# Performance work log

Hardware: AMD Instinct MI355X
Metric: run time of the kernel (lower is better)

## Reference

```python
import jax, jax.numpy as jnp
import numpy as np

N_NODES = 100000
N_EDGES = 1200000
NFEAT, NHID, NCLASS = 64, 256, 40
DROP_RATE = 0.5
ORDER = 8


def setup_inputs() -> dict:
    key = jax.random.key(0)
    k = jax.random.split(key, 6)
    x = jax.random.normal(k[0], (N_NODES, NFEAT), dtype=jnp.float32)
    edge_index = jax.random.randint(k[1], (2, N_EDGES), 0, N_NODES, dtype=jnp.int64)
    stdv1 = 1.0 / np.sqrt(NHID)
    stdv2 = 1.0 / np.sqrt(NCLASS)
    W1 = jax.random.normal(k[2], (NFEAT, NHID), dtype=jnp.float32) * stdv1
    b1 = jax.random.normal(k[3], (NHID,), dtype=jnp.float32) * stdv1
    W2 = jax.random.normal(k[4], (NHID, NCLASS), dtype=jnp.float32) * stdv2
    b2 = jax.random.normal(k[5], (NCLASS,), dtype=jnp.float32) * stdv2
    return {"x": x, "edge_index": edge_index, "W1": W1, "b1": b1, "W2": W2, "b2": b2}


def _norm_adj(edge_index, n):
    # A + I, then D^{-1/2} (A+I) D^{-1/2}  (GCN symmetric normalization)
    loops = jnp.arange(n, dtype=edge_index.dtype)
    row = jnp.concatenate([edge_index[0], loops])
    col = jnp.concatenate([edge_index[1], loops])
    ones = jnp.ones(row.shape[0], dtype=jnp.float32)
    deg = jax.ops.segment_sum(ones, row, num_segments=n)  # row sums (self-loops guarantee deg>=1)
    d_inv_sqrt = 1.0 / jnp.sqrt(deg)
    ew = d_inv_sqrt[row] * d_inv_sqrt[col]  # [E+N] edge weights
    return row, col, ew


def reference(x, edge_index, W1, b1, W2, b2):
    n = x.shape[0]
    row, col, ew = _norm_adj(edge_index, n)

    def spmm(h):  # out[row] += ew * h[col]
        return jax.ops.segment_sum(ew[:, None] * h[col], row, num_segments=n)

    # eval-mode input scaling (training=False branch of GRAND.forward)
    h = x * (1.0 - DROP_RATE)
    y = h
    for _ in range(ORDER):
        h = spmm(h)
        y = y + h
    y = y / (ORDER + 1.0)

    # MLP in eval mode: dropouts are no-ops, use_bn=False
    hid = jax.nn.relu(y @ W1 + b1)
    return hid @ W2 + b2
```

## Files before the change

kernel.cpp:

```cpp
#include <hip/hip_runtime.h>

#define NN 100000
#define NE 1200000
#define NF 64
#define NH 256
#define NC 40
#define ORDER_C 8
#define BINB 1024
#define BCAP 165000
#define NSB 782
#define SBROWS 128
#define SBCAP 1920
#define NLB 100
#define CCAP (NE + 7 * NN)

typedef __attribute__((ext_vector_type(8))) short short8;
typedef __attribute__((ext_vector_type(4))) float f32x4;

__device__ __forceinline__ unsigned bf16r(float x) {
    unsigned u = __float_as_uint(x);
    return (u + 0x7FFFu + ((u >> 16) & 1u)) >> 16;
}
__device__ __forceinline__ unsigned packbf(float lo, float hi) {
    return bf16r(lo) | (bf16r(hi) << 16);
}
__device__ __forceinline__ float bflo(unsigned u) { return __uint_as_float(u << 16); }
__device__ __forceinline__ float bfhi(unsigned u) { return __uint_as_float(u & 0xFFFF0000u); }


static __global__ __launch_bounds__(256) void k_bin(const int* __restrict__ rows,
                                                    const int* __restrict__ cols,
                                                    int* __restrict__ bcnt,
                                                    int* __restrict__ browb,
                                                    int* __restrict__ bcolb, int E)
{
    __shared__ int rbuf[BINB];
    __shared__ unsigned short lofs[BINB];
    __shared__ int hist[8], basew[8];
    int t = threadIdx.x;
    int e0 = blockIdx.x * BINB;
    int m = E - e0; if (m > BINB) m = BINB;
    if (t < 8) hist[t] = 0;
    __syncthreads();
    for (int i = t; i < m; i += 256) {
        int r = rows[e0 + i];
        rbuf[i] = r;
        int b = r / 12500;
        lofs[i] = (unsigned short)atomicAdd(&hist[b], 1);
    }
    __syncthreads();
    if (t < 8) basew[t] = atomicAdd(&bcnt[t], hist[t]);
    __syncthreads();
    for (int i = t; i < m; i += 256) {
        int r = rbuf[i];
        int b = r / 12500;
        size_t pos = (size_t)b * BCAP + basew[b] + lofs[i];
        browb[pos] = r;
        bcolb[pos] = cols[e0 + i];
    }
}


static __global__ __launch_bounds__(256) void k_bin98(const int* __restrict__ browb,
                                                      const int* __restrict__ bcolb,
                                                      const int* __restrict__ bcnt,
                                                      int* __restrict__ sbcnt,
                                                      int* __restrict__ sbrow,
                                                      int* __restrict__ sbcol)
{
    __shared__ int rbuf[2048];
    __shared__ unsigned short lofs[2048];
    __shared__ int hist[NLB], basew[NLB];
    int t = threadIdx.x;
    int b = blockIdx.x & 7;
    int m = bcnt[b];
    int lo_sb = (b * 12500) >> 7;
    const int* srcr = browb + (size_t)b * BCAP;
    const int* srcc = bcolb + (size_t)b * BCAP;
    int stride = (gridDim.x >> 3) * 2048;
    for (int base = (blockIdx.x >> 3) * 2048; base < m; base += stride) {
        int cm = m - base; if (cm > 2048) cm = 2048;
        if (t < NLB) hist[t] = 0;
        __syncthreads();
        for (int i = t; i < cm; i += 256) {
            int r = srcr[base + i];
            rbuf[i] = r;
            lofs[i] = (unsigned short)atomicAdd(&hist[(r >> 7) - lo_sb], 1);
        }
        __syncthreads();
        if (t < NLB) {
            int h = hist[t];
            basew[t] = h ? atomicAdd(&sbcnt[lo_sb + t], h) : 0;
        }
        __syncthreads();
        for (int i = t; i < cm; i += 256) {
            int r = rbuf[i];
            int sb = r >> 7;
            int pos = sb * SBCAP + basew[sb - lo_sb] + lofs[i];
            sbrow[pos] = r;
            sbcol[pos] = srcc[base + i];
        }
        __syncthreads();
    }
}


static __global__ __launch_bounds__(256) void k_hist(const int* __restrict__ sbrow,
                                                     const int* __restrict__ sbcnt,
                                                     int* __restrict__ ghist,
                                                     int* __restrict__ sbtot)
{
    __shared__ int h[SBROWS];
    __shared__ int red[256];
    int sb = blockIdx.x;
    int t = threadIdx.x;
    int m = sbcnt[sb];
    const int* src = sbrow + (size_t)sb * SBCAP;
    if (t < SBROWS) h[t] = 0;
    __syncthreads();
    for (int i = t; i < m; i += 256) atomicAdd(&h[src[i] & 127], 1);
    __syncthreads();
    int pad = 0;
    if (t < SBROWS) {
        ghist[sb * SBROWS + t] = h[t];
        pad = (h[t] + 7) & ~7;
    }
    red[t] = pad;
    __syncthreads();
    for (int off = 128; off > 0; off >>= 1) {
        if (t < off) red[t] += red[t + off];
        __syncthreads();
    }
    if (t == 0) sbtot[sb] = red[0];
}


static __global__ __launch_bounds__(1024) void k_scansb(const int* __restrict__ sbtot,
                                                        int* __restrict__ sbbase,
                                                        int* __restrict__ rp, int n)
{
    __shared__ int red[1024];
    int t = threadIdx.x;
    int v = (t < NSB) ? sbtot[t] : 0;
    red[t] = v;
    __syncthreads();
    for (int off = 1; off < 1024; off <<= 1) {
        int x = (t >= off) ? red[t - off] : 0;
        __syncthreads();
        red[t] += x;
        __syncthreads();
    }
    if (t < NSB) sbbase[t] = (t == 0) ? 0 : red[t - 1];
    if (t == NSB - 1) rp[n] = red[t];
}


static __global__ __launch_bounds__(256) void k_csr(const int* __restrict__ sbrow,
                                                    const int* __restrict__ sbcol,
                                                    const int* __restrict__ sbcnt,
                                                    const int* __restrict__ ghist,
                                                    const int* __restrict__ sbbase,
                                                    int* __restrict__ rp,
                                                    float2* __restrict__ drd,
                                                    int* __restrict__ ccol, int n)
{
    __shared__ int rb[SBCAP];
    __shared__ int cb[SBCAP];
    __shared__ int sc[SBROWS], ro[SBROWS], fl[SBROWS];
    int sb = blockIdx.x;
    int t = threadIdx.x;
    int m = sbcnt[sb];
    const int* srcr = sbrow + (size_t)sb * SBCAP;
    const int* srcc = sbcol + (size_t)sb * SBCAP;
    for (int i = t; i < m; i += 256) { rb[i] = srcr[i] & 127; cb[i] = srcc[i]; }
    int h = (t < SBROWS) ? ghist[sb * SBROWS + t] : 0;
    if (t < SBROWS) { sc[t] = (h + 7) & ~7; fl[t] = 0; }
    __syncthreads();
    for (int off = 1; off < SBROWS; off <<= 1) {
        int x = (t >= off && t < SBROWS) ? sc[t - off] : 0;
        __syncthreads();
        if (t < SBROWS) sc[t] += x;
        __syncthreads();
    }
    int base = sbbase[sb];
    if (t < SBROWS) {
        ro[t] = (t == 0) ? 0 : sc[t - 1];
        int row = sb * SBROWS + t;
        if (row < n) {
            rp[row] = base + ro[t];
            float d1 = rsqrtf((float)(h + 1));
            drd[row] = make_float2(d1, (float)(h + 1) * d1);
            int p = (h + 7) & ~7;
            for (int q = h; q < p; ++q) ccol[base + ro[t] + q] = n;
        }
    }
    __syncthreads();
    for (int i = t; i < m; i += 256) {
        int r = rb[i];
        int rank = atomicAdd(&fl[r], 1);
        ccol[base + ro[r] + rank] = cb[i];
    }
}


static __global__ __launch_bounds__(256) void k_pack(const float* __restrict__ W1,
                                                     const float* __restrict__ W2,
                                                     unsigned short* __restrict__ w1f,
                                                     unsigned short* __restrict__ w2f)
{
    int t = blockIdx.x * 256 + threadIdx.x;
    if (t < 2048) {
        int lane = t & 63;
        int g = lane >> 4, col = (lane & 15) + ((t >> 6) & 15) * 16;
        int s = t >> 10;
        unsigned short* p = w1f + (size_t)t * 8;
        #pragma unroll
        for (int e = 0; e < 8; ++e) {
            int k = 32 * s + 8 * g + e;
            p[e] = (unsigned short)bf16r(W1[k * NH + col]);
        }
    } else if (t < 2048 + 1536) {
        int u = t - 2048;
        int lane = u & 63;
        int tile = u >> 6;
        int nt = tile % 3, s = tile / 3;
        int g = lane >> 4, col = (lane & 15) + nt * 16;
        unsigned short* p = w2f + (size_t)u * 8;
        #pragma unroll
        for (int e = 0; e < 8; ++e) {
            int k = 32 * s + 8 * g + e;
            p[e] = (col < NC) ? (unsigned short)bf16r(W2[k * NC + col]) : 0;
        }
    }
}


static __global__ __launch_bounds__(256) void k_init(const float4* __restrict__ x4,
                                                     float4* __restrict__ y4,
                                                     uint4* __restrict__ ga,
                                                     uint4* __restrict__ gbp,
                                                     const float2* __restrict__ drd,
                                                     int nchunk)
{
    int i = blockIdx.x * 256 + threadIdx.x;
    if (i >= nchunk) {
        if (i < nchunk + 8) {
            uint4 z = make_uint4(0, 0, 0, 0);
            ga[i] = z; gbp[i] = z;
        }
        return;
    }
    float d1 = drd[i >> 3].x;
    float4 a = x4[i * 2], b = x4[i * 2 + 1];
    a.x *= 0.5f; a.y *= 0.5f; a.z *= 0.5f; a.w *= 0.5f;
    b.x *= 0.5f; b.y *= 0.5f; b.z *= 0.5f; b.w *= 0.5f;
    y4[i * 2] = a; y4[i * 2 + 1] = b;
    ga[i] = make_uint4(packbf(a.x * d1, a.y * d1), packbf(a.z * d1, a.w * d1),
                       packbf(b.x * d1, b.y * d1), packbf(b.z * d1, b.w * d1));
}


template<bool ACC, bool WRITEG>
static __global__ __launch_bounds__(256) void k_spmm(const uint2* __restrict__ gb,
                                                     uint2* __restrict__ go,
                                                     float4* __restrict__ y4,
                                                     const int* __restrict__ rp,
                                                     const int* __restrict__ ccol,
                                                     const float2* __restrict__ drd, int n)
{
    int wid  = (blockIdx.x * 256 + threadIdx.x) >> 6;
    int lane = threadIdx.x & 63;
    int row  = wid * 4 + (lane >> 4);
    int j    = lane & 15;
    if (row >= n) return;
    int s = rp[row], e = rp[row + 1];

    float a0 = 0.f, a1 = 0.f, a2 = 0.f, a3 = 0.f;
    float b0 = 0.f, b1 = 0.f, b2 = 0.f, b3 = 0.f;
    for (int i = s; i < e; i += 8) {
        int4 cA = *(const int4*)&ccol[i];
        int4 cB = *(const int4*)&ccol[i + 4];
        uint2 h0 = gb[(size_t)cA.x * 16 + j];
        uint2 h1 = gb[(size_t)cA.y * 16 + j];
        uint2 h2 = gb[(size_t)cA.z * 16 + j];
        uint2 h3 = gb[(size_t)cA.w * 16 + j];
        uint2 h4 = gb[(size_t)cB.x * 16 + j];
        uint2 h5 = gb[(size_t)cB.y * 16 + j];
        uint2 h6 = gb[(size_t)cB.z * 16 + j];
        uint2 h7 = gb[(size_t)cB.w * 16 + j];
        a0 += bflo(h0.x); a1 += bfhi(h0.x); a2 += bflo(h0.y); a3 += bfhi(h0.y);
        b0 += bflo(h1.x); b1 += bfhi(h1.x); b2 += bflo(h1.y); b3 += bfhi(h1.y);
        a0 += bflo(h2.x); a1 += bfhi(h2.x); a2 += bflo(h2.y); a3 += bfhi(h2.y);
        b0 += bflo(h3.x); b1 += bfhi(h3.x); b2 += bflo(h3.y); b3 += bfhi(h3.y);
        a0 += bflo(h4.x); a1 += bfhi(h4.x); a2 += bflo(h4.y); a3 += bfhi(h4.y);
        b0 += bflo(h5.x); b1 += bfhi(h5.x); b2 += bflo(h5.y); b3 += bfhi(h5.y);
        a0 += bflo(h6.x); a1 += bfhi(h6.x); a2 += bflo(h6.y); a3 += bfhi(h6.y);
        b0 += bflo(h7.x); b1 += bfhi(h7.x); b2 += bflo(h7.y); b3 += bfhi(h7.y);
    }

    float2 dr = drd[row];
    uint2 gs = gb[(size_t)row * 16 + j];
    float g0 = bflo(gs.x), g1 = bfhi(gs.x), g2 = bflo(gs.y), g3 = bfhi(gs.y);
    float s0 = (a0 + b0) + g0;
    float s1 = (a1 + b1) + g1;
    float s2 = (a2 + b2) + g2;
    float s3 = (a3 + b3) + g3;
    float h0 = dr.x * s0, h1 = dr.x * s1, h2 = dr.x * s2, h3 = dr.x * s3;
    if (WRITEG)
        go[(size_t)row * 16 + j] = make_uint2(packbf(dr.x * h0, dr.x * h1),
                                              packbf(dr.x * h2, dr.x * h3));
    if (ACC) {
        float4 yv = y4[(size_t)row * 16 + j];
        yv.x += fmaf(g0, dr.y, h0);
        yv.y += fmaf(g1, dr.y, h1);
        yv.z += fmaf(g2, dr.y, h2);
        yv.w += fmaf(g3, dr.y, h3);
        y4[(size_t)row * 16 + j] = yv;
    }
}


#define YSTR 72
#define HSTR 264

static __global__ __launch_bounds__(256) void k_mlp(const float4* __restrict__ y4,
                                                    const short8* __restrict__ w1f,
                                                    const short8* __restrict__ w2f,
                                                    const float* __restrict__ b1,
                                                    const float* __restrict__ b2,
                                                    float* __restrict__ out, int n)
{
    __shared__ short lds[64 * HSTR];
    int t = threadIdx.x;
    int lane = t & 63;
    int w = t >> 6;
    int base = blockIdx.x * 64;
    const float S = 1.f / 9.f;

    {
        int r = t >> 2, q = t & 3;
        int row = base + r;
        unsigned v[8];
        if (row < n) {
            const float4* yp = y4 + (size_t)row * 16 + q * 4;
            #pragma unroll
            for (int i = 0; i < 4; ++i) {
                float4 f = yp[i];
                v[i * 2]     = packbf(f.x * S, f.y * S);
                v[i * 2 + 1] = packbf(f.z * S, f.w * S);
            }
        } else {
            #pragma unroll
            for (int i = 0; i < 8; ++i) v[i] = 0;
        }
        uint4* dst = (uint4*)&lds[r * YSTR + q * 16];
        dst[0] = make_uint4(v[0], v[1], v[2], v[3]);
        dst[1] = make_uint4(v[4], v[5], v[6], v[7]);
    }
    __syncthreads();

    int m = lane & 15, g = lane >> 4;

    f32x4 acc[4][4];
    {
        short8 a[4][2];
        #pragma unroll
        for (int mt = 0; mt < 4; ++mt)
            #pragma unroll
            for (int s = 0; s < 2; ++s)
                a[mt][s] = *(const short8*)&lds[(mt * 16 + m) * YSTR + s * 32 + g * 8];
        #pragma unroll
        for (int nt4 = 0; nt4 < 4; ++nt4) {
            int nt = w * 4 + nt4;
            short8 b0  = w1f[nt * 64 + lane];
            short8 b1v = w1f[(16 + nt) * 64 + lane];
            float bias = b1[nt * 16 + m];
            #pragma unroll
            for (int mt = 0; mt < 4; ++mt) {
                f32x4 c = {bias, bias, bias, bias};
                c = __builtin_amdgcn_mfma_f32_16x16x32_bf16(a[mt][0], b0,  c, 0, 0, 0);
                c = __builtin_amdgcn_mfma_f32_16x16x32_bf16(a[mt][1], b1v, c, 0, 0, 0);
                acc[mt][nt4] = c;
            }
        }
    }
    __syncthreads();

    {
        #pragma unroll
        for (int mt = 0; mt < 4; ++mt)
            #pragma unroll
            for (int nt4 = 0; nt4 < 4; ++nt4) {
                int col = w * 64 + nt4 * 16 + m;
                #pragma unroll
                for (int r = 0; r < 4; ++r) {
                    float hv = fmaxf(acc[mt][nt4][r], 0.f);
                    lds[(mt * 16 + g * 4 + r) * HSTR + col] = (short)bf16r(hv);
                }
            }
    }
    __syncthreads();

    {
        short8 a2[8];
        #pragma unroll
        for (int s = 0; s < 8; ++s)
            a2[s] = *(const short8*)&lds[(w * 16 + m) * HSTR + s * 32 + g * 8];
        #pragma unroll
        for (int nt = 0; nt < 3; ++nt) {
            int col = nt * 16 + m;
            float bias = (col < NC) ? b2[col] : 0.f;
            f32x4 c = {bias, bias, bias, bias};
            #pragma unroll
            for (int s = 0; s < 8; ++s)
                c = __builtin_amdgcn_mfma_f32_16x16x32_bf16(a2[s], w2f[(s * 3 + nt) * 64 + lane], c, 0, 0, 0);
            if (col < NC) {
                #pragma unroll
                for (int r = 0; r < 4; ++r) {
                    int row = base + w * 16 + g * 4 + r;
                    if (row < n) out[(size_t)row * NC + col] = c[r];
                }
            }
        }
    }
}


extern "C" void kernel_launch(void* const* d_in, const int* in_sizes, int n_in,
                              void* d_out, int out_size, void* d_ws, size_t ws_size,
                              hipStream_t stream)
{
    const float* x  = (const float*)d_in[0];
    const int*   ei = (const int*)d_in[1];
    const float* W1 = (const float*)d_in[2];
    const float* b1 = (const float*)d_in[3];
    const float* W2 = (const float*)d_in[4];
    const float* b2 = (const float*)d_in[5];
    float* out = (float*)d_out;

    const int n = NN, E = NE;

    char* ws = (char*)d_ws;
    size_t off = 0;
    auto alloc = [&](size_t bytes) -> void* {
        void* p = ws + off;
        off = (off + bytes + 255) & ~(size_t)255;
        return p;
    };
    int*    rp     = (int*)   alloc((size_t)(n + 1) * 4);
    float2* drd    = (float2*)alloc((size_t)n * 8);
    int*    bcnt   = (int*)   alloc(8 * 4);
    int*    sbcnt  = (int*)   alloc(NSB * 4);
    int*    sbtot  = (int*)   alloc(NSB * 4);
    int*    sbbase = (int*)   alloc(NSB * 4);
    int*    browb  = (int*)   alloc((size_t)8 * BCAP * 4);
    int*    bcolb  = (int*)   alloc((size_t)8 * BCAP * 4);
    int*    sbrow  = (int*)   alloc((size_t)NSB * SBCAP * 4);
    int*    sbcol  = (int*)   alloc((size_t)NSB * SBCAP * 4);
    int*    ghist  = (int*)   alloc((size_t)NSB * SBROWS * 4);
    int*    ccol   = (int*)   alloc((size_t)CCAP * 4);
    unsigned short* w1f = (unsigned short*)alloc(2048 * 8 * 2);
    unsigned short* w2f = (unsigned short*)alloc(1536 * 8 * 2);
    uint4* ha   = (uint4*)alloc((size_t)(n + 1) * NF * 2);
    uint4* hbuf = (uint4*)alloc((size_t)(n + 1) * NF * 2);
    float* y    = (float*)alloc((size_t)n * NF * 4);

    hipMemsetAsync(bcnt, 0, 8 * 4, stream);
    hipMemsetAsync(sbcnt, 0, NSB * 4, stream);

    const int* rows = ei;
    const int* cols = ei + E;

    k_bin   <<<(E + BINB - 1) / BINB, 256, 0, stream>>>(rows, cols, bcnt, browb, bcolb, E);
    k_bin98 <<<640, 256, 0, stream>>>(browb, bcolb, bcnt, sbcnt, sbrow, sbcol);
    k_hist  <<<NSB, 256, 0, stream>>>(sbrow, sbcnt, ghist, sbtot);
    k_scansb<<<1, 1024, 0, stream>>>(sbtot, sbbase, rp, n);
    k_csr   <<<NSB, 256, 0, stream>>>(sbrow, sbcol, sbcnt, ghist, sbbase, rp, drd, ccol, n);
    k_pack  <<<14, 256, 0, stream>>>(W1, W2, w1f, w2f);

    int nchunk = n * 8;
    k_init<<<(nchunk + 8 + 255) / 256, 256, 0, stream>>>((const float4*)x, (float4*)y,
                                                         ha, hbuf, drd, nchunk);

    uint4* cur = ha;
    uint4* nxt = hbuf;
    int spmm_blocks = (n + 15) / 16;
    for (int it = 0; it < ORDER_C; ++it) {
        bool acc = (it & 1) != 0;
        bool wg  = (it != ORDER_C - 1);
        if (acc && wg)
            k_spmm<true, true><<<spmm_blocks, 256, 0, stream>>>((const uint2*)cur, (uint2*)nxt,
                                                                (float4*)y, rp, ccol, drd, n);
        else if (acc)
            k_spmm<true, false><<<spmm_blocks, 256, 0, stream>>>((const uint2*)cur, (uint2*)nxt,
                                                                 (float4*)y, rp, ccol, drd, n);
        else
            k_spmm<false, true><<<spmm_blocks, 256, 0, stream>>>((const uint2*)cur, (uint2*)nxt,
                                                                 (float4*)y, rp, ccol, drd, n);
        uint4* tswap = cur; cur = nxt; nxt = tswap;
    }

    k_mlp<<<(n + 63) / 64, 256, 0, stream>>>((const float4*)y, (const short8*)w1f,
                                             (const short8*)w2f, b1, b2, out, n);
}
```

Before: 327.6 us.

## Split feature dimension into two halves and run SpMM propagation per half

The bf16 propagated features are stored as two separate 32-feature planes, each 64 bytes per row, and the eight SpMM iterations run twice, once per half. Each half's gather working set (about 6.4 MB) is half the size of the full one, so it is more likely to stay in L2/MALL cache during the random neighbour gathers. In exchange, kernel launches double, the CSR index arrays are read twice, and each gather is only 64 bytes per neighbour.

```diff
diff --git a/kernel.cpp b/kernel.cpp
--- a/kernel.cpp
+++ b/kernel.cpp
@@ -237,16 +237,19 @@
 
 static __global__ __launch_bounds__(256) void k_init(const float4* __restrict__ x4,
                                                      float4* __restrict__ y4,
-                                                     uint4* __restrict__ ga,
-                                                     uint4* __restrict__ gbp,
+                                                     uint2* __restrict__ ga,
+                                                     uint2* __restrict__ gbp,
                                                      const float2* __restrict__ drd,
                                                      int nchunk)
 {
     int i = blockIdx.x * 256 + threadIdx.x;
     if (i >= nchunk) {
-        if (i < nchunk + 8) {
-            uint4 z = make_uint4(0, 0, 0, 0);
-            ga[i] = z; gbp[i] = z;
+        int extra = i - nchunk;
+        if (extra < 32) {
+            uint2* buf = (extra & 16) ? gbp : ga;
+            int k = extra & 15;
+            int half = k >> 3, slot = k & 7;
+            buf[(size_t)half * (NN + 1) * 8 + (size_t)NN * 8 + slot] = make_uint2(0u, 0u);
         }
         return;
     }
@@ -255,23 +258,26 @@
     a.x *= 0.5f; a.y *= 0.5f; a.z *= 0.5f; a.w *= 0.5f;
     b.x *= 0.5f; b.y *= 0.5f; b.z *= 0.5f; b.w *= 0.5f;
     y4[i * 2] = a; y4[i * 2 + 1] = b;
-    ga[i] = make_uint4(packbf(a.x * d1, a.y * d1), packbf(a.z * d1, a.w * d1),
-                       packbf(b.x * d1, b.y * d1), packbf(b.z * d1, b.w * d1));
+    int row = i >> 3, q = i & 7;
+    int half = q >> 2, slot2 = (q & 3) * 2;
+    uint4* dst = (uint4*)&ga[(size_t)half * (NN + 1) * 8 + (size_t)row * 8 + slot2];
+    *dst = make_uint4(packbf(a.x * d1, a.y * d1), packbf(a.z * d1, a.w * d1),
+                      packbf(b.x * d1, b.y * d1), packbf(b.z * d1, b.w * d1));
 }
 
 
 template<bool ACC, bool WRITEG>
-static __global__ __launch_bounds__(256) void k_spmm(const uint2* __restrict__ gb,
-                                                     uint2* __restrict__ go,
-                                                     float4* __restrict__ y4,
-                                                     const int* __restrict__ rp,
-                                                     const int* __restrict__ ccol,
-                                                     const float2* __restrict__ drd, int n)
+static __global__ __launch_bounds__(256) void k_spmm_h(const uint2* __restrict__ gb,
+                                                       uint2* __restrict__ go,
+                                                       float4* __restrict__ yh,
+                                                       const int* __restrict__ rp,
+                                                       const int* __restrict__ ccol,
+                                                       const float2* __restrict__ drd, int n)
 {
     int wid  = (blockIdx.x * 256 + threadIdx.x) >> 6;
     int lane = threadIdx.x & 63;
-    int row  = wid * 4 + (lane >> 4);
-    int j    = lane & 15;
+    int row  = wid * 8 + (lane >> 3);
+    int j    = lane & 7;
     if (row >= n) return;
     int s = rp[row], e = rp[row + 1];
 
@@ -280,14 +286,14 @@
     for (int i = s; i < e; i += 8) {
         int4 cA = *(const int4*)&ccol[i];
         int4 cB = *(const int4*)&ccol[i + 4];
-        uint2 h0 = gb[(size_t)cA.x * 16 + j];
-        uint2 h1 = gb[(size_t)cA.y * 16 + j];
-        uint2 h2 = gb[(size_t)cA.z * 16 + j];
-        uint2 h3 = gb[(size_t)cA.w * 16 + j];
-        uint2 h4 = gb[(size_t)cB.x * 16 + j];
-        uint2 h5 = gb[(size_t)cB.y * 16 + j];
-        uint2 h6 = gb[(size_t)cB.z * 16 + j];
-        uint2 h7 = gb[(size_t)cB.w * 16 + j];
+        uint2 h0 = gb[(size_t)cA.x * 8 + j];
+        uint2 h1 = gb[(size_t)cA.y * 8 + j];
+        uint2 h2 = gb[(size_t)cA.z * 8 + j];
+        uint2 h3 = gb[(size_t)cA.w * 8 + j];
+        uint2 h4 = gb[(size_t)cB.x * 8 + j];
+        uint2 h5 = gb[(size_t)cB.y * 8 + j];
+        uint2 h6 = gb[(size_t)cB.z * 8 + j];
+        uint2 h7 = gb[(size_t)cB.w * 8 + j];
         a0 += bflo(h0.x); a1 += bfhi(h0.x); a2 += bflo(h0.y); a3 += bfhi(h0.y);
         b0 += bflo(h1.x); b1 += bfhi(h1.x); b2 += bflo(h1.y); b3 += bfhi(h1.y);
         a0 += bflo(h2.x); a1 += bfhi(h2.x); a2 += bflo(h2.y); a3 += bfhi(h2.y);
@@ -299,7 +305,7 @@
     }
 
     float2 dr = drd[row];
-    uint2 gs = gb[(size_t)row * 16 + j];
+    uint2 gs = gb[(size_t)row * 8 + j];
     float g0 = bflo(gs.x), g1 = bfhi(gs.x), g2 = bflo(gs.y), g3 = bfhi(gs.y);
     float s0 = (a0 + b0) + g0;
     float s1 = (a1 + b1) + g1;
@@ -307,15 +313,15 @@
     float s3 = (a3 + b3) + g3;
     float h0 = dr.x * s0, h1 = dr.x * s1, h2 = dr.x * s2, h3 = dr.x * s3;
     if (WRITEG)
-        go[(size_t)row * 16 + j] = make_uint2(packbf(dr.x * h0, dr.x * h1),
-                                              packbf(dr.x * h2, dr.x * h3));
+        go[(size_t)row * 8 + j] = make_uint2(packbf(dr.x * h0, dr.x * h1),
+                                             packbf(dr.x * h2, dr.x * h3));
     if (ACC) {
-        float4 yv = y4[(size_t)row * 16 + j];
+        float4 yv = yh[(size_t)row * 16 + j];
         yv.x += fmaf(g0, dr.y, h0);
         yv.y += fmaf(g1, dr.y, h1);
         yv.z += fmaf(g2, dr.y, h2);
         yv.w += fmaf(g3, dr.y, h3);
-        y4[(size_t)row * 16 + j] = yv;
+        yh[(size_t)row * 16 + j] = yv;
     }
 }
 
@@ -461,8 +467,8 @@
     int*    ccol   = (int*)   alloc((size_t)CCAP * 4);
     unsigned short* w1f = (unsigned short*)alloc(2048 * 8 * 2);
     unsigned short* w2f = (unsigned short*)alloc(1536 * 8 * 2);
-    uint4* ha   = (uint4*)alloc((size_t)(n + 1) * NF * 2);
-    uint4* hbuf = (uint4*)alloc((size_t)(n + 1) * NF * 2);
+    uint2* gA   = (uint2*)alloc((size_t)2 * (n + 1) * 8 * 8);
+    uint2* gB   = (uint2*)alloc((size_t)2 * (n + 1) * 8 * 8);
     float* y    = (float*)alloc((size_t)n * NF * 4);
 
     hipMemsetAsync(bcnt, 0, 8 * 4, stream);
@@ -479,25 +485,29 @@
     k_pack  <<<14, 256, 0, stream>>>(W1, W2, w1f, w2f);
 
     int nchunk = n * 8;
-    k_init<<<(nchunk + 8 + 255) / 256, 256, 0, stream>>>((const float4*)x, (float4*)y,
-                                                         ha, hbuf, drd, nchunk);
-
-    uint4* cur = ha;
-    uint4* nxt = hbuf;
-    int spmm_blocks = (n + 15) / 16;
-    for (int it = 0; it < ORDER_C; ++it) {
-        bool acc = (it & 1) != 0;
-        bool wg  = (it != ORDER_C - 1);
-        if (acc && wg)
-            k_spmm<true, true><<<spmm_blocks, 256, 0, stream>>>((const uint2*)cur, (uint2*)nxt,
-                                                                (float4*)y, rp, ccol, drd, n);
-        else if (acc)
-            k_spmm<true, false><<<spmm_blocks, 256, 0, stream>>>((const uint2*)cur, (uint2*)nxt,
-                                                                 (float4*)y, rp, ccol, drd, n);
-        else
-            k_spmm<false, true><<<spmm_blocks, 256, 0, stream>>>((const uint2*)cur, (uint2*)nxt,
-                                                                 (float4*)y, rp, ccol, drd, n);
-        uint4* tswap = cur; cur = nxt; nxt = tswap;
+    k_init<<<(nchunk + 32 + 255) / 256, 256, 0, stream>>>((const float4*)x, (float4*)y,
+                                                          gA, gB, drd, nchunk);
+
+    const size_t HSTRIDE = (size_t)(NN + 1) * 8;
+    int spmm_blocks = (n + 31) / 32;
+    for (int half = 0; half < 2; ++half) {
+        uint2* cur = gA + (size_t)half * HSTRIDE;
+        uint2* nxt = gB + (size_t)half * HSTRIDE;
+        float4* yh = (float4*)y + half * 8;
+        for (int it = 0; it < ORDER_C; ++it) {
+            bool acc = (it & 1) != 0;
+            bool wg  = (it != ORDER_C - 1);
+            if (acc && wg)
+                k_spmm_h<true, true><<<spmm_blocks, 256, 0, stream>>>(cur, nxt, yh,
+                                                                      rp, ccol, drd, n);
+            else if (acc)
+                k_spmm_h<true, false><<<spmm_blocks, 256, 0, stream>>>(cur, nxt, yh,
+                                                                       rp, ccol, drd, n);
+            else
+                k_spmm_h<false, true><<<spmm_blocks, 256, 0, stream>>>(cur, nxt, yh,
+                                                                       rp, ccol, drd, n);
+            uint2* tswap = cur; cur = nxt; nxt = tswap;
+        }
     }
 
     k_mlp<<<(n + 63) / 64, 256, 0, stream>>>((const float4*)y, (const short8*)w1f,
```

Result: slower. 407.1 us (+24.3%).
